# Performance work log

Measured on AMD Instinct MI355X. Metric: run time of the kernel, lower is better.

Reference implementation:

```python
import jax, jax.numpy as jnp
import numpy as np
from jax import lax

N = 120000      # total real voxels
C = 128         # d_model
NH = 8          # heads
HD = C // NH    # head dim
T = 36          # window capacity
FILL = 24       # real tokens per window
NW = N // FILL  # 5000 windows
L = 4           # encoder layers (num_blocks=2, 2 layers each)
DFF = 256
B, H, Wd = 2, 320, 320
SCALE = HD ** -0.5


def setup_inputs() -> dict:
    key = jax.random.key(0)
    ks = jax.random.split(key, 16)
    voxel_feats = jax.random.normal(ks[0], (N, C), jnp.float32)
    # shift-0 window assignment: contiguous; shift-1: random permutation of voxels
    base = jnp.arange(N, dtype=jnp.int32)
    ind0 = (base // FILL) * T + (base % FILL)
    perm = jax.random.permutation(ks[1], N).astype(jnp.int32)
    ind1 = (perm // FILL) * T + (perm % FILL)
    mask = jnp.tile(jnp.arange(T) >= FILL, (NW, 1))  # True = padded key slot
    pos0 = 0.02 * jax.random.normal(ks[2], (NW, T, C), jnp.float32)
    pos1 = 0.02 * jax.random.normal(ks[3], (NW, T, C), jnp.float32)
    bcol = (jnp.arange(N) >= N // 2).astype(jnp.int32)
    yy = jax.random.randint(ks[4], (N,), 0, H, jnp.int32)
    xx = jax.random.randint(ks[5], (N,), 0, Wd, jnp.int32)
    voxel_coors = jnp.stack([bcol, jnp.zeros(N, jnp.int32), yy, xx], axis=1)
    s = 0.02
    return dict(
        voxel_feats=voxel_feats,
        pos0=pos0, pos1=pos1,
        in_proj_w=s * jax.random.normal(ks[6], (L, 3 * C, C), jnp.float32),
        in_proj_b=jnp.zeros((L, 3 * C), jnp.float32),
        out_proj_w=s * jax.random.normal(ks[7], (L, C, C), jnp.float32),
        out_proj_b=jnp.zeros((L, C), jnp.float32),
        lin1_w=s * jax.random.normal(ks[8], (L, DFF, C), jnp.float32),
        lin1_b=jnp.zeros((L, DFF), jnp.float32),
        lin2_w=s * jax.random.normal(ks[9], (L, C, DFF), jnp.float32),
        lin2_b=jnp.zeros((L, C), jnp.float32),
        ln1_w=jnp.ones((L, C), jnp.float32), ln1_b=jnp.zeros((L, C), jnp.float32),
        ln2_w=jnp.ones((L, C), jnp.float32), ln2_b=jnp.zeros((L, C), jnp.float32),
        conv_w=0.05 * jax.random.normal(ks[10], (2, C, C, 3, 3), jnp.float32),
        voxel_coors=voxel_coors, ind0=ind0, ind1=ind1, mask0=mask, mask1=mask,
    )


def _ln(x, w, b):
    m = jnp.mean(x, -1, keepdims=True)
    v = jnp.mean((x - m) ** 2, -1, keepdims=True)
    return (x - m) * lax.rsqrt(v + 1e-5) * w + b


def _encoder_layer(x, ind, pos, mask, ipw, ipb, opw, opb, l1w, l1b, l2w, l2b,
                   n1w, n1b, n2w, n2b):
    # flat2window_v2: scatter flat tokens into padded window buffer
    feat3d = jnp.zeros((NW * T, C), x.dtype).at[ind].set(x).reshape(NW, T, C)
    qk_in = feat3d + pos  # pos added to q and k only
    wq, wk, wv = ipw[:C], ipw[C:2 * C], ipw[2 * C:]
    bq, bk, bv = ipb[:C], ipb[C:2 * C], ipb[2 * C:]
    q = (qk_in @ wq.T + bq).reshape(NW, T, NH, HD)
    k = (qk_in @ wk.T + bk).reshape(NW, T, NH, HD)
    v = (feat3d @ wv.T + bv).reshape(NW, T, NH, HD)
    scores = jnp.einsum('wqhd,wkhd->whqk', q, k) * SCALE
    scores = jnp.where(mask[:, None, None, :], -1e9, scores)  # key padding mask
    attn = jax.nn.softmax(scores, axis=-1)
    o = jnp.einsum('whqk,wkhd->wqhd', attn, v).reshape(NW, T, C)
    o = o @ opw.T + opb
    a = o.reshape(NW * T, C)[ind]  # window2flat_v2: gather valid slots
    x = _ln(x + a, n1w, n1b)       # post_norm residual 1
    f = jax.nn.gelu(x @ l1w.T + l1b, approximate=False) @ l2w.T + l2b
    return _ln(x + f, n2w, n2b)    # post_norm residual 2


def reference(voxel_feats, pos0, pos1, in_proj_w, in_proj_b, out_proj_w,
              out_proj_b, lin1_w, lin1_b, lin2_w, lin2_b, ln1_w, ln1_b,
              ln2_w, ln2_b, conv_w, voxel_coors, ind0, ind1, mask0, mask1):
    x = voxel_feats
    for l in range(L):
        ind, pos, mask = (ind0, pos0, mask0) if l % 2 == 0 else (ind1, pos1, mask1)
        x = _encoder_layer(x, ind, pos, mask, in_proj_w[l], in_proj_b[l],
                           out_proj_w[l], out_proj_b[l], lin1_w[l], lin1_b[l],
                           lin2_w[l], lin2_b[l], ln1_w[l], ln1_b[l],
                           ln2_w[l], ln2_b[l])
    # recover_bev: scatter tokens into dense [B, C, H, W] canvas
    flat = voxel_coors[:, 2] * Wd + voxel_coors[:, 3]
    canvas = jnp.zeros((B, H * Wd, C), x.dtype).at[voxel_coors[:, 0], flat].set(x)
    out = canvas.reshape(B, H, Wd, C).transpose(0, 3, 1, 2)
    for i in range(2):  # attached 3x3 conv (bias=False) + ReLU
        out = jax.nn.relu(lax.conv_general_dilated(
            out, conv_w[i], (1, 1), [(1, 1), (1, 1)],
            dimension_numbers=('NCHW', 'OIHW', 'NCHW')))
    return out
```

## Files before the change

### kernel.cpp

```cpp
#include <hip/hip_runtime.h>
#include <math.h>

#define NVOX 120000
#define CDIM 128
#define NWIN 5000
#define HWPIX 102400
#define PW 322
#define PCELLS 103684

typedef __attribute__((ext_vector_type(8))) short short8;
typedef __attribute__((ext_vector_type(4))) float f32x4;

__device__ __forceinline__ unsigned short f2bf(float f) {
  unsigned u = __float_as_uint(f);
  return (unsigned short)((u + 0x7FFFu + ((u >> 16) & 1u)) >> 16);
}
__device__ __forceinline__ unsigned pack2(float a, float b) {
  return (unsigned)f2bf(a) | ((unsigned)f2bf(b) << 16);
}
__device__ __forceinline__ void unpack2(unsigned u, float& a, float& b) {
  a = __uint_as_float(u << 16);
  b = __uint_as_float(u & 0xFFFF0000u);
}

__device__ __forceinline__ void mma128(const short* __restrict__ As,
                                       const short* __restrict__ Ws,
                                       int aoff, int boff, f32x4 acc[2][4]) {
#pragma unroll
  for (int kc = 0; kc < 4; ++kc) {
    short8 a0 = *(const short8*)(As + aoff + kc * 32);
    short8 a1 = *(const short8*)(As + aoff + 136 * 16 + kc * 32);
#pragma unroll
    for (int nt = 0; nt < 4; ++nt) {
      short8 b = *(const short8*)(Ws + boff + nt * 136 * 16 + kc * 32);
      acc[0][nt] = __builtin_amdgcn_mfma_f32_16x16x32_bf16(a0, b, acc[0][nt], 0, 0, 0);
      acc[1][nt] = __builtin_amdgcn_mfma_f32_16x16x32_bf16(a1, b, acc[1][nt], 0, 0, 0);
    }
  }
}

__global__ __launch_bounds__(256) void cvt_kernel(const float* __restrict__ src,
                                                  unsigned short* __restrict__ dst, int n4) {
  int i = blockIdx.x * 256 + threadIdx.x;
  if (i >= n4) return;
  float4 v = ((const float4*)src)[i];
  uint2 o; o.x = pack2(v.x, v.y); o.y = pack2(v.z, v.w);
  ((uint2*)dst)[i] = o;
}

__global__ __launch_bounds__(256) void cvtT_kernel(const float* __restrict__ w,
                                                   unsigned short* __restrict__ wT) {
  int idx = blockIdx.x * 256 + threadIdx.x;
  if (idx >= 2 * 9 * 128 * 128) return;
  int ci = idx & 127;
  int co = (idx >> 7) & 127;
  int tap = (idx >> 14) % 9;
  int conv = idx / (9 * 16384);
  wT[idx] = f2bf(w[((size_t)(conv * 128 + co) * 128 + ci) * 9 + tap]);
}

__global__ __launch_bounds__(256) void qkv_kernel(
    const unsigned short* __restrict__ x, const float* __restrict__ pos,
    const int* __restrict__ ind, const unsigned short* __restrict__ ipwB,
    const float* __restrict__ ipb, unsigned short* __restrict__ qb,
    unsigned short* __restrict__ kb, unsigned short* __restrict__ vb) {
  __shared__ __align__(16) char ldsraw[52224];
  short* As = (short*)ldsraw;
  short* Ws = (short*)(ldsraw + 17408);
  const int t = threadIdx.x;
  const int lane = t & 63, wv = t >> 6;
  const int l15 = lane & 15, quad = lane >> 4;
  const int rbase = 32 * (wv >> 1), cbase = 64 * (wv & 1);
  const int mbase = blockIdx.x * 64;
  const int sec = blockIdx.y;
  f32x4 acc[2][4];
#pragma unroll
  for (int m = 0; m < 2; ++m)
#pragma unroll
    for (int n = 0; n < 4; ++n) acc[m][n] = (f32x4){0.f, 0.f, 0.f, 0.f};

  for (int fi = t; fi < 1024; fi += 256) {
    int row = fi >> 4, c8 = fi & 15;
    int vox = mbase + row;
    uint4 xv = ((const uint4*)x)[(size_t)vox * 16 + c8];
    if (sec < 2) {
      int s = ind[vox];
      const float4* pp = (const float4*)(pos + (size_t)s * 128 + c8 * 8);
      float4 p0 = pp[0], p1 = pp[1];
      float f0, f1, f2, f3, f4, f5, f6, f7;
      unpack2(xv.x, f0, f1); unpack2(xv.y, f2, f3);
      unpack2(xv.z, f4, f5); unpack2(xv.w, f6, f7);
      xv.x = pack2(f0 + p0.x, f1 + p0.y); xv.y = pack2(f2 + p0.z, f3 + p0.w);
      xv.z = pack2(f4 + p1.x, f5 + p1.y); xv.w = pack2(f6 + p1.z, f7 + p1.w);
    }
    *(uint4*)&As[row * 136 + c8 * 8] = xv;
  }
  for (int fi = t; fi < 2048; fi += 256) {
    int row = fi >> 4, c8 = fi & 15;
    ((uint4*)&Ws[row * 136])[c8] =
        ((const uint4*)(ipwB + (size_t)(sec * 128 + row) * 128))[c8];
  }
  __syncthreads();
  mma128(As, Ws, (rbase + l15) * 136 + quad * 8, (cbase + l15) * 136 + quad * 8, acc);
  __syncthreads();

  short* Ybf = (short*)ldsraw;
#pragma unroll
  for (int nt = 0; nt < 4; ++nt) {
    int col = cbase + nt * 16 + l15;
    float bias = ipb[sec * 128 + col];
#pragma unroll
    for (int mt = 0; mt < 2; ++mt)
#pragma unroll
      for (int r = 0; r < 4; ++r)
        Ybf[(rbase + mt * 16 + quad * 4 + r) * 136 + col] =
            (short)f2bf(acc[mt][nt][r] + bias);
  }
  __syncthreads();
  unsigned short* dst = (sec == 0) ? qb : ((sec == 1) ? kb : vb);
  for (int fi = t; fi < 1024; fi += 256) {
    int row = fi >> 4, c8 = fi & 15;
    int s = ind[mbase + row];
    int slot = (s / 36) * 24 + (s % 36);
    ((uint4*)dst)[(size_t)slot * 16 + c8] = ((const uint4*)&Ybf[row * 136])[c8];
  }
}

__global__ __launch_bounds__(256) void attn_kernel(
    unsigned short* __restrict__ qb, const unsigned short* __restrict__ kb,
    const unsigned short* __restrict__ vb) {
  __shared__ float lds[14112];
  float* Qs = lds;
  float* Ks = lds + 3168;
  float* Vs = lds + 6336;
  float* S = lds + 9504;
  const int t = threadIdx.x;
  const size_t base = (size_t)blockIdx.x * 3072;
  for (int fi = t; fi < 1152; fi += 256) {
    int arr = fi / 384, rem = fi % 384;
    int row = rem >> 4, c8 = rem & 15;
    const unsigned short* src = arr == 0 ? qb : (arr == 1 ? kb : vb);
    uint4 raw = ((const uint4*)(src + base))[row * 16 + c8];
    float* dl = lds + arr * 3168 + row * 132 + c8 * 8;
    unpack2(raw.x, dl[0], dl[1]); unpack2(raw.y, dl[2], dl[3]);
    unpack2(raw.z, dl[4], dl[5]); unpack2(raw.w, dl[6], dl[7]);
  }
  __syncthreads();
  for (int idx = t; idx < 4608; idx += 256) {
    int hh = idx / 576, rem = idx % 576;
    int qq = rem / 24, kk = rem % 24;
    const float* qp = &Qs[qq * 132 + hh * 16];
    const float* kp = &Ks[kk * 132 + hh * 16];
    float s = 0.f;
#pragma unroll
    for (int d = 0; d < 16; ++d) s = fmaf(qp[d], kp[d], s);
    S[idx] = s * 0.25f;
  }
  __syncthreads();
  if (t < 192) {
    float* rowp = &S[t * 24];
    float m = rowp[0];
#pragma unroll
    for (int k2 = 1; k2 < 24; ++k2) m = fmaxf(m, rowp[k2]);
    float sum = 0.f;
#pragma unroll
    for (int k2 = 0; k2 < 24; ++k2) { float e = __expf(rowp[k2] - m); rowp[k2] = e; sum += e; }
    float inv = 1.f / sum;
#pragma unroll
    for (int k2 = 0; k2 < 24; ++k2) rowp[k2] *= inv;
  }
  __syncthreads();
  for (int idx = t; idx < 3072; idx += 256) {
    int hh = idx / 384, rem = idx % 384;
    int qq = rem >> 4, dd = rem & 15;
    const float* pp = &S[hh * 576 + qq * 24];
    const float* vp = &Vs[hh * 16 + dd];
    float o = 0.f;
#pragma unroll
    for (int k2 = 0; k2 < 24; ++k2) o = fmaf(pp[k2], vp[k2 * 132], o);
    qb[base + qq * 128 + hh * 16 + dd] = f2bf(o);
  }
}

__global__ __launch_bounds__(256) void outln_kernel(
    const unsigned short* __restrict__ o, const int* __restrict__ ind,
    const unsigned short* __restrict__ opwB, const float* __restrict__ opb,
    const unsigned short* __restrict__ xres, const float* __restrict__ lnw,
    const float* __restrict__ lnb, unsigned short* __restrict__ hout) {
  __shared__ __align__(16) char ldsraw[52224];
  short* As = (short*)ldsraw;
  short* Ws = (short*)(ldsraw + 17408);
  const int t = threadIdx.x;
  const int lane = t & 63, wv = t >> 6;
  const int l15 = lane & 15, quad = lane >> 4;
  const int rbase = 32 * (wv >> 1), cbase = 64 * (wv & 1);
  const int mbase = blockIdx.x * 64;
  f32x4 acc[2][4];
#pragma unroll
  for (int m = 0; m < 2; ++m)
#pragma unroll
    for (int n = 0; n < 4; ++n) acc[m][n] = (f32x4){0.f, 0.f, 0.f, 0.f};

  for (int fi = t; fi < 1024; fi += 256) {
    int row = fi >> 4, c8 = fi & 15;
    int s = ind[mbase + row];
    int slot = (s / 36) * 24 + (s % 36);
    *(uint4*)&As[row * 136 + c8 * 8] = ((const uint4*)o)[(size_t)slot * 16 + c8];
  }
  for (int fi = t; fi < 2048; fi += 256) {
    int row = fi >> 4, c8 = fi & 15;
    ((uint4*)&Ws[row * 136])[c8] = ((const uint4*)(opwB + (size_t)row * 128))[c8];
  }
  __syncthreads();
  mma128(As, Ws, (rbase + l15) * 136 + quad * 8, (cbase + l15) * 136 + quad * 8, acc);
  __syncthreads();

  float* Yf = (float*)ldsraw;
  float* p1 = (float*)(ldsraw + 33792);
  float* p2 = (float*)(ldsraw + 34816);
  float* Ms = (float*)(ldsraw + 35840);
  float* Rs = (float*)(ldsraw + 36096);
#pragma unroll
  for (int nt = 0; nt < 4; ++nt) {
    int col = cbase + nt * 16 + l15;
    float bias = opb[col];
#pragma unroll
    for (int mt = 0; mt < 2; ++mt)
#pragma unroll
      for (int r = 0; r < 4; ++r)
        Yf[(rbase + mt * 16 + quad * 4 + r) * 132 + col] = acc[mt][nt][r] + bias;
  }
  __syncthreads();
  for (int fi = t; fi < 1024; fi += 256) {
    int row = fi >> 4, c8 = fi & 15;
    uint4 xv = ((const uint4*)xres)[(size_t)(mbase + row) * 16 + c8];
    float* yp = &Yf[row * 132 + c8 * 8];
    float a, b;
    unpack2(xv.x, a, b); yp[0] += a; yp[1] += b;
    unpack2(xv.y, a, b); yp[2] += a; yp[3] += b;
    unpack2(xv.z, a, b); yp[4] += a; yp[5] += b;
    unpack2(xv.w, a, b); yp[6] += a; yp[7] += b;
  }
  __syncthreads();
  {
    int r = t & 63, g = t >> 6;
    float s = 0.f, s2 = 0.f;
    for (int c = g * 32; c < g * 32 + 32; ++c) { float v = Yf[r * 132 + c]; s += v; s2 += v * v; }
    p1[g * 64 + r] = s; p2[g * 64 + r] = s2;
  }
  __syncthreads();
  if (t < 64) {
    float s = p1[t] + p1[64 + t] + p1[128 + t] + p1[192 + t];
    float s2 = p2[t] + p2[64 + t] + p2[128 + t] + p2[192 + t];
    float m = s * (1.f / 128.f);
    float var = s2 * (1.f / 128.f) - m * m;
    Ms[t] = m; Rs[t] = rsqrtf(var + 1e-5f);
  }
  __syncthreads();
  for (int fi = t; fi < 1024; fi += 256) {
    int row = fi >> 4, c8 = fi & 15;
    float m = Ms[row], rr = Rs[row];
    const float* yp = &Yf[row * 132 + c8 * 8];
    uint4 ov;
    float v0, v1;
#define LNPAIR(J, FLD) \
    v0 = (yp[2*J] - m) * rr * lnw[c8*8+2*J] + lnb[c8*8+2*J]; \
    v1 = (yp[2*J+1] - m) * rr * lnw[c8*8+2*J+1] + lnb[c8*8+2*J+1]; \
    ov.FLD = pack2(v0, v1);
    LNPAIR(0, x) LNPAIR(1, y) LNPAIR(2, z) LNPAIR(3, w)
#undef LNPAIR
    ((uint4*)hout)[(size_t)(mbase + row) * 16 + c8] = ov;
  }
}

__global__ __launch_bounds__(256) void ffn1_kernel(
    const unsigned short* __restrict__ h, const unsigned short* __restrict__ w1B,
    const float* __restrict__ b1, unsigned short* __restrict__ ff) {
  __shared__ __align__(16) char ldsraw[52224];
  short* As = (short*)ldsraw;
  short* Ws = (short*)(ldsraw + 17408);
  const int t = threadIdx.x;
  const int lane = t & 63, wv = t >> 6;
  const int l15 = lane & 15, quad = lane >> 4;
  const int rbase = 32 * (wv >> 1), cbase = 64 * (wv & 1);
  const int mbase = blockIdx.x * 64;
  const int by = blockIdx.y;
  f32x4 acc[2][4];
#pragma unroll
  for (int m = 0; m < 2; ++m)
#pragma unroll
    for (int n = 0; n < 4; ++n) acc[m][n] = (f32x4){0.f, 0.f, 0.f, 0.f};

  for (int fi = t; fi < 1024; fi += 256) {
    int row = fi >> 4, c8 = fi & 15;
    *(uint4*)&As[row * 136 + c8 * 8] = ((const uint4*)h)[(size_t)(mbase + row) * 16 + c8];
  }
  for (int fi = t; fi < 2048; fi += 256) {
    int row = fi >> 4, c8 = fi & 15;
    ((uint4*)&Ws[row * 136])[c8] =
        ((const uint4*)(w1B + (size_t)(by * 128 + row) * 128))[c8];
  }
  __syncthreads();
  mma128(As, Ws, (rbase + l15) * 136 + quad * 8, (cbase + l15) * 136 + quad * 8, acc);
  __syncthreads();

  short* Ybf = (short*)ldsraw;
#pragma unroll
  for (int nt = 0; nt < 4; ++nt) {
    int col = cbase + nt * 16 + l15;
    float bias = b1[by * 128 + col];
#pragma unroll
    for (int mt = 0; mt < 2; ++mt)
#pragma unroll
      for (int r = 0; r < 4; ++r) {
        float v = acc[mt][nt][r] + bias;
        float g = 0.5f * v * (1.f + erff(v * 0.70710678f));
        Ybf[(rbase + mt * 16 + quad * 4 + r) * 136 + col] = (short)f2bf(g);
      }
  }
  __syncthreads();
  for (int fi = t; fi < 1024; fi += 256) {
    int row = fi >> 4, c8 = fi & 15;
    ((uint4*)ff)[(size_t)(mbase + row) * 32 + by * 16 + c8] =
        ((const uint4*)&Ybf[row * 136])[c8];
  }
}

__global__ __launch_bounds__(256) void ffn2_kernel(
    const unsigned short* __restrict__ ff, const unsigned short* __restrict__ w2B,
    const float* __restrict__ b2, const unsigned short* __restrict__ hres,
    const float* __restrict__ lnw, const float* __restrict__ lnb,
    unsigned short* __restrict__ xout) {
  __shared__ __align__(16) char ldsraw[52224];
  short* As = (short*)ldsraw;
  short* Ws = (short*)(ldsraw + 17408);
  const int t = threadIdx.x;
  const int lane = t & 63, wv = t >> 6;
  const int l15 = lane & 15, quad = lane >> 4;
  const int rbase = 32 * (wv >> 1), cbase = 64 * (wv & 1);
  const int mbase = blockIdx.x * 64;
  f32x4 acc[2][4];
#pragma unroll
  for (int m = 0; m < 2; ++m)
#pragma unroll
    for (int n = 0; n < 4; ++n) acc[m][n] = (f32x4){0.f, 0.f, 0.f, 0.f};

  for (int k2 = 0; k2 < 2; ++k2) {
    if (k2) __syncthreads();
    for (int fi = t; fi < 1024; fi += 256) {
      int row = fi >> 4, c8 = fi & 15;
      *(uint4*)&As[row * 136 + c8 * 8] =
          ((const uint4*)ff)[(size_t)(mbase + row) * 32 + k2 * 16 + c8];
    }
    for (int fi = t; fi < 2048; fi += 256) {
      int row = fi >> 4, c8 = fi & 15;
      ((uint4*)&Ws[row * 136])[c8] =
          ((const uint4*)(w2B + (size_t)row * 256 + k2 * 128))[c8];
    }
    __syncthreads();
    mma128(As, Ws, (rbase + l15) * 136 + quad * 8, (cbase + l15) * 136 + quad * 8, acc);
  }
  __syncthreads();

  float* Yf = (float*)ldsraw;
  float* p1 = (float*)(ldsraw + 33792);
  float* p2 = (float*)(ldsraw + 34816);
  float* Ms = (float*)(ldsraw + 35840);
  float* Rs = (float*)(ldsraw + 36096);
#pragma unroll
  for (int nt = 0; nt < 4; ++nt) {
    int col = cbase + nt * 16 + l15;
    float bias = b2[col];
#pragma unroll
    for (int mt = 0; mt < 2; ++mt)
#pragma unroll
      for (int r = 0; r < 4; ++r)
        Yf[(rbase + mt * 16 + quad * 4 + r) * 132 + col] = acc[mt][nt][r] + bias;
  }
  __syncthreads();
  for (int fi = t; fi < 1024; fi += 256) {
    int row = fi >> 4, c8 = fi & 15;
    uint4 xv = ((const uint4*)hres)[(size_t)(mbase + row) * 16 + c8];
    float* yp = &Yf[row * 132 + c8 * 8];
    float a, b;
    unpack2(xv.x, a, b); yp[0] += a; yp[1] += b;
    unpack2(xv.y, a, b); yp[2] += a; yp[3] += b;
    unpack2(xv.z, a, b); yp[4] += a; yp[5] += b;
    unpack2(xv.w, a, b); yp[6] += a; yp[7] += b;
  }
  __syncthreads();
  {
    int r = t & 63, g = t >> 6;
    float s = 0.f, s2 = 0.f;
    for (int c = g * 32; c < g * 32 + 32; ++c) { float v = Yf[r * 132 + c]; s += v; s2 += v * v; }
    p1[g * 64 + r] = s; p2[g * 64 + r] = s2;
  }
  __syncthreads();
  if (t < 64) {
    float s = p1[t] + p1[64 + t] + p1[128 + t] + p1[192 + t];
    float s2 = p2[t] + p2[64 + t] + p2[128 + t] + p2[192 + t];
    float m = s * (1.f / 128.f);
    float var = s2 * (1.f / 128.f) - m * m;
    Ms[t] = m; Rs[t] = rsqrtf(var + 1e-5f);
  }
  __syncthreads();
  for (int fi = t; fi < 1024; fi += 256) {
    int row = fi >> 4, c8 = fi & 15;
    float m = Ms[row], rr = Rs[row];
    const float* yp = &Yf[row * 132 + c8 * 8];
    uint4 ov;
    float v0, v1;
#define LNPAIR(J, FLD) \
    v0 = (yp[2*J] - m) * rr * lnw[c8*8+2*J] + lnb[c8*8+2*J]; \
    v1 = (yp[2*J+1] - m) * rr * lnw[c8*8+2*J+1] + lnb[c8*8+2*J+1]; \
    ov.FLD = pack2(v0, v1);
    LNPAIR(0, x) LNPAIR(1, y) LNPAIR(2, z) LNPAIR(3, w)
#undef LNPAIR
    ((uint4*)xout)[(size_t)(mbase + row) * 16 + c8] = ov;
  }
}

__global__ void idx_init_kernel(int* __restrict__ idxmap) {
  int i = blockIdx.x * 256 + threadIdx.x;
  if (i < 2 * HWPIX) idxmap[i] = -1;
}

__global__ void scatter_kernel(const int* __restrict__ coors, int* __restrict__ idxmap) {
  int i = blockIdx.x * 256 + threadIdx.x;
  if (i >= NVOX) return;
  int b = coors[i * 4 + 0], y = coors[i * 4 + 2], xx = coors[i * 4 + 3];
  atomicMax(&idxmap[b * HWPIX + y * 320 + xx], i);
}

__global__ void canvas_kernel(const unsigned short* __restrict__ x,
                              const int* __restrict__ idxmap,
                              unsigned short* __restrict__ canvas) {
  int idx = blockIdx.x * 256 + threadIdx.x;
  if (idx >= 2 * PCELLS * 16) return;
  int cell = idx >> 4, c8 = idx & 15;
  int b = (cell >= PCELLS) ? 1 : 0;
  cell -= b * PCELLS;
  int yy = cell / PW, xx = cell - yy * PW;
  uint4 v = {0u, 0u, 0u, 0u};
  if (yy >= 1 && yy <= 320 && xx >= 1 && xx <= 320) {
    int vox = idxmap[b * HWPIX + (yy - 1) * 320 + (xx - 1)];
    if (vox >= 0) v = ((const uint4*)x)[(size_t)vox * 16 + c8];
  }
  ((uint4*)canvas)[idx] = v;
}

__global__ void border_kernel(unsigned short* __restrict__ buf) {
  int i = blockIdx.x * 256 + threadIdx.x;
  if (i >= 2 * 1284 * 16) return;
  int c8 = i & 15, j = i >> 4;
  int b = (j >= 1284) ? 1 : 0;
  j -= b * 1284;
  int cell;
  if (j < 322) cell = j;
  else if (j < 644) cell = 321 * PW + (j - 322);
  else { int j2 = j - 644; cell = (1 + (j2 >> 1)) * PW + (j2 & 1) * 321; }
  uint4 z = {0u, 0u, 0u, 0u};
  ((uint4*)buf)[((size_t)b * PCELLS + cell) * 16 + c8] = z;
}

template <int NCHW_OUT>
__global__ __launch_bounds__(256) void conv_kernel(
    const unsigned short* __restrict__ in, const unsigned short* __restrict__ wTb,
    void* __restrict__ outp) {
  __shared__ __align__(16) char ldsraw[67584];
  const int t = threadIdx.x;
  const int lane = t & 63, wv = t >> 6;
  const int l15 = lane & 15, quad = lane >> 4;
  const int wr = wv >> 1, wc = wv & 1;
  const int x0 = blockIdx.x * 64;
  const int y0 = blockIdx.y * 2;
  const int b = blockIdx.z;
  const unsigned short* inb = in + (size_t)b * PCELLS * 128;
  const int srow = t >> 4, sc8 = t & 15;

  f32x4 acc[4][4];
#pragma unroll
  for (int m = 0; m < 4; ++m)
#pragma unroll
    for (int n = 0; n < 4; ++n) acc[m][n] = (f32x4){0.f, 0.f, 0.f, 0.f};

  uint4 wreg[8];
#pragma unroll
  for (int i = 0; i < 8; ++i)
    wreg[i] = ((const uint4*)(wTb + (size_t)(i * 16 + srow) * 128))[sc8];
  {
    short* W0 = (short*)ldsraw;
#pragma unroll
    for (int i = 0; i < 8; ++i)
      *(uint4*)&W0[(i * 16 + srow) * 132 + sc8 * 8] = wreg[i];
  }
  __syncthreads();

#pragma unroll
  for (int tap = 0; tap < 9; ++tap) {
    const int dy = tap / 3, dx = tap % 3;
    const short* Wcur = (const short*)(ldsraw + (tap & 1) * 33792);
    if (tap < 8) {
#pragma unroll
      for (int i = 0; i < 8; ++i)
        wreg[i] = ((const uint4*)(wTb + (size_t)((tap + 1) * 128 + i * 16 + srow) * 128))[sc8];
    }
    const unsigned short* ap =
        inb + (size_t)((y0 + wr + dy) * PW + x0 + dx + l15) * 128 + quad * 8;
    const short* bp = Wcur + (wc * 64 + l15) * 132 + quad * 8;
#pragma unroll
    for (int kc = 0; kc < 4; ++kc) {
      short8 av[4], bvv[4];
#pragma unroll
      for (int mt = 0; mt < 4; ++mt)
        av[mt] = *(const short8*)(ap + mt * 16 * 128 + kc * 32);
#pragma unroll
      for (int nt = 0; nt < 4; ++nt)
        bvv[nt] = *(const short8*)(bp + nt * 16 * 132 + kc * 32);
#pragma unroll
      for (int mt = 0; mt < 4; ++mt)
#pragma unroll
        for (int nt = 0; nt < 4; ++nt)
          acc[mt][nt] = __builtin_amdgcn_mfma_f32_16x16x32_bf16(av[mt], bvv[nt], acc[mt][nt], 0, 0, 0);
    }
    if (tap < 8) {
      short* Wnxt = (short*)(ldsraw + ((tap + 1) & 1) * 33792);
#pragma unroll
      for (int i = 0; i < 8; ++i)
        *(uint4*)&Wnxt[(i * 16 + srow) * 132 + sc8 * 8] = wreg[i];
      __syncthreads();
    }
  }
  __syncthreads();

  if (NCHW_OUT) {
    float* Yf = (float*)ldsraw;
#pragma unroll
    for (int nt = 0; nt < 4; ++nt) {
      int co = wc * 64 + nt * 16 + l15;
#pragma unroll
      for (int mt = 0; mt < 4; ++mt)
#pragma unroll
        for (int r = 0; r < 4; ++r)
          Yf[co * 129 + wr * 64 + mt * 16 + quad * 4 + r] = fmaxf(acc[mt][nt][r], 0.f);
    }
    __syncthreads();
    float* out = (float*)outp;
    for (int fi = t; fi < 4096; fi += 256) {
      int co = fi >> 5, q4 = fi & 31;
      int px = q4 * 4;
      int yy = y0 + (px >> 6), xx = x0 + (px & 63);
      *(float4*)&out[(size_t)(b * 128 + co) * HWPIX + yy * 320 + xx] =
          *(const float4*)&Yf[co * 129 + px];
    }
  } else {
    short* Ybf = (short*)ldsraw;
#pragma unroll
    for (int nt = 0; nt < 4; ++nt) {
      int co = wc * 64 + nt * 16 + l15;
#pragma unroll
      for (int mt = 0; mt < 4; ++mt)
#pragma unroll
        for (int r = 0; r < 4; ++r)
          Ybf[(wr * 64 + mt * 16 + quad * 4 + r) * 132 + co] =
              (short)f2bf(fmaxf(acc[mt][nt][r], 0.f));
    }
    __syncthreads();
    unsigned short* out = (unsigned short*)outp;
    for (int fi = t; fi < 2048; fi += 256) {
      int row = fi >> 4, c8 = fi & 15;
      int yy = y0 + (row >> 6) + 1, xx = x0 + (row & 63) + 1;
      ((uint4*)out)[((size_t)b * PCELLS + yy * PW + xx) * 16 + c8] =
          ((const uint4*)&Ybf[row * 132])[c8];
    }
  }
}

extern "C" void kernel_launch(void* const* d_in, const int* in_sizes, int n_in,
                              void* d_out, int out_size, void* d_ws, size_t ws_size,
                              hipStream_t stream) {
  const float* voxel_feats = (const float*)d_in[0];
  const float* pos0 = (const float*)d_in[1];
  const float* pos1 = (const float*)d_in[2];
  const float* ipw = (const float*)d_in[3];
  const float* ipb = (const float*)d_in[4];
  const float* opw = (const float*)d_in[5];
  const float* opb = (const float*)d_in[6];
  const float* l1w = (const float*)d_in[7];
  const float* l1b = (const float*)d_in[8];
  const float* l2w = (const float*)d_in[9];
  const float* l2b = (const float*)d_in[10];
  const float* n1w = (const float*)d_in[11];
  const float* n1b = (const float*)d_in[12];
  const float* n2w = (const float*)d_in[13];
  const float* n2b = (const float*)d_in[14];
  const float* convw = (const float*)d_in[15];
  const int* coors = (const int*)d_in[16];
  const int* ind0 = (const int*)d_in[17];
  const int* ind1 = (const int*)d_in[18];

  unsigned short* ws = (unsigned short*)d_ws;
  const size_t NC = (size_t)NVOX * CDIM;
  unsigned short* bx = ws;
  unsigned short* bq = ws + NC;
  unsigned short* bk = ws + 2 * NC;
  unsigned short* bv = ws + 3 * NC;
  unsigned short* bh = ws + 4 * NC;
  unsigned short* bff = ws + 5 * NC;
  unsigned short* wB = ws + 7 * NC;
  unsigned short* ipwB = wB;
  unsigned short* opwB = wB + 196608;
  unsigned short* l1wB = wB + 262144;
  unsigned short* l2wB = wB + 393216;
  unsigned short* convB = wB + 524288;
  int* idxmap = (int*)(wB + 819200);
  unsigned short* canvas = bq;
  unsigned short* c1out = bv;

  cvt_kernel<<<15000, 256, 0, stream>>>(voxel_feats, bx, 3840000);
  cvt_kernel<<<192, 256, 0, stream>>>(ipw, ipwB, 49152);
  cvt_kernel<<<64, 256, 0, stream>>>(opw, opwB, 16384);
  cvt_kernel<<<128, 256, 0, stream>>>(l1w, l1wB, 32768);
  cvt_kernel<<<128, 256, 0, stream>>>(l2w, l2wB, 32768);
  cvtT_kernel<<<1152, 256, 0, stream>>>(convw, convB);

  for (int l = 0; l < 4; ++l) {
    const int* ind = (l & 1) ? ind1 : ind0;
    const float* pos = (l & 1) ? pos1 : pos0;
    qkv_kernel<<<dim3(1875, 3), 256, 0, stream>>>(
        bx, pos, ind, ipwB + (size_t)l * 49152, ipb + l * 384, bq, bk, bv);
    attn_kernel<<<NWIN, 256, 0, stream>>>(bq, bk, bv);
    outln_kernel<<<1875, 256, 0, stream>>>(
        bq, ind, opwB + (size_t)l * 16384, opb + l * 128, bx,
        n1w + l * 128, n1b + l * 128, bh);
    ffn1_kernel<<<dim3(1875, 2), 256, 0, stream>>>(
        bh, l1wB + (size_t)l * 32768, l1b + l * 256, bff);
    ffn2_kernel<<<1875, 256, 0, stream>>>(
        bff, l2wB + (size_t)l * 32768, l2b + l * 128, bh,
        n2w + l * 128, n2b + l * 128, bx);
  }

  idx_init_kernel<<<800, 256, 0, stream>>>(idxmap);
  scatter_kernel<<<(NVOX + 255) / 256, 256, 0, stream>>>(coors, idxmap);
  canvas_kernel<<<(2 * PCELLS * 16 + 255) / 256, 256, 0, stream>>>(bx, idxmap, canvas);
  border_kernel<<<(2 * 1284 * 16 + 255) / 256, 256, 0, stream>>>(c1out);

  conv_kernel<0><<<dim3(5, 160, 2), 256, 0, stream>>>(canvas, convB, (void*)c1out);
  conv_kernel<1><<<dim3(5, 160, 2), 256, 0, stream>>>(c1out, convB + 9 * 16384, d_out);
}
```

Baseline: 1.759 ms.

## Stage conv input row patch in LDS and tile one output row per block

The 3x3 conv kernel now loads a 66-pixel input row patch into shared memory and reuses it across the three horizontal taps, refreshing it only when the tap row changes. Before, A operands were read straight from global memory for every tap. Each block now covers one output row instead of two, and the grid doubles. Weights move to a single LDS buffer, so an extra barrier is needed per tap. The cost is more blocks that each redo the weight loading, which halves weight reuse per block. The diff calls an mma128 helper that it does not show being defined.

```diff
diff --git a/kernel.cpp b/kernel.cpp
--- a/kernel.cpp
+++ b/kernel.cpp
@@ -467,111 +467,119 @@
 __global__ __launch_bounds__(256) void conv_kernel(
     const unsigned short* __restrict__ in, const unsigned short* __restrict__ wTb,
     void* __restrict__ outp) {
-  __shared__ __align__(16) char ldsraw[67584];
+  __shared__ __align__(16) char ldsraw[52768];
+  short* patch = (short*)ldsraw;
+  short* Wt = (short*)(ldsraw + 17952);
   const int t = threadIdx.x;
   const int lane = t & 63, wv = t >> 6;
   const int l15 = lane & 15, quad = lane >> 4;
-  const int wr = wv >> 1, wc = wv & 1;
+  const int rbase = 32 * (wv >> 1), cbase = 64 * (wv & 1);
   const int x0 = blockIdx.x * 64;
-  const int y0 = blockIdx.y * 2;
+  const int y0 = blockIdx.y;
   const int b = blockIdx.z;
   const unsigned short* inb = in + (size_t)b * PCELLS * 128;
   const int srow = t >> 4, sc8 = t & 15;
 
-  f32x4 acc[4][4];
-#pragma unroll
-  for (int m = 0; m < 4; ++m)
+  f32x4 acc[2][4];
+#pragma unroll
+  for (int m = 0; m < 2; ++m)
 #pragma unroll
     for (int n = 0; n < 4; ++n) acc[m][n] = (f32x4){0.f, 0.f, 0.f, 0.f};
 
   uint4 wreg[8];
+  uint4 pp[4], px4;
+
+  {
+    const uint4* src = (const uint4*)inb + ((size_t)y0 * PW + x0) * 16;
+#pragma unroll
+    for (int k = 0; k < 4; ++k) pp[k] = src[t + 256 * k];
+    if (t < 32) px4 = src[1024 + t];
+  }
 #pragma unroll
   for (int i = 0; i < 8; ++i)
     wreg[i] = ((const uint4*)(wTb + (size_t)(i * 16 + srow) * 128))[sc8];
-  {
-    short* W0 = (short*)ldsraw;
-#pragma unroll
-    for (int i = 0; i < 8; ++i)
-      *(uint4*)&W0[(i * 16 + srow) * 132 + sc8 * 8] = wreg[i];
-  }
+#pragma unroll
+  for (int k = 0; k < 4; ++k) {
+    int e = t + 256 * k;
+    *(uint4*)&patch[(e >> 4) * 136 + (e & 15) * 8] = pp[k];
+  }
+  if (t < 32) { int e = 1024 + t; *(uint4*)&patch[(e >> 4) * 136 + (e & 15) * 8] = px4; }
+#pragma unroll
+  for (int i = 0; i < 8; ++i)
+    *(uint4*)&Wt[(i * 16 + srow) * 136 + sc8 * 8] = wreg[i];
   __syncthreads();
 
 #pragma unroll
   for (int tap = 0; tap < 9; ++tap) {
     const int dy = tap / 3, dx = tap % 3;
-    const short* Wcur = (const short*)(ldsraw + (tap & 1) * 33792);
-    if (tap < 8) {
+    const bool pfP = (dx == 2) && (dy < 2);
+    const bool pfW = (tap < 8);
+    if (pfP) {
+      const uint4* src = (const uint4*)inb + ((size_t)(y0 + dy + 1) * PW + x0) * 16;
+#pragma unroll
+      for (int k = 0; k < 4; ++k) pp[k] = src[t + 256 * k];
+      if (t < 32) px4 = src[1024 + t];
+    }
+    if (pfW) {
 #pragma unroll
       for (int i = 0; i < 8; ++i)
         wreg[i] = ((const uint4*)(wTb + (size_t)((tap + 1) * 128 + i * 16 + srow) * 128))[sc8];
     }
-    const unsigned short* ap =
-        inb + (size_t)((y0 + wr + dy) * PW + x0 + dx + l15) * 128 + quad * 8;
-    const short* bp = Wcur + (wc * 64 + l15) * 132 + quad * 8;
-#pragma unroll
-    for (int kc = 0; kc < 4; ++kc) {
-      short8 av[4], bvv[4];
-#pragma unroll
-      for (int mt = 0; mt < 4; ++mt)
-        av[mt] = *(const short8*)(ap + mt * 16 * 128 + kc * 32);
-#pragma unroll
-      for (int nt = 0; nt < 4; ++nt)
-        bvv[nt] = *(const short8*)(bp + nt * 16 * 132 + kc * 32);
-#pragma unroll
-      for (int mt = 0; mt < 4; ++mt)
-#pragma unroll
-        for (int nt = 0; nt < 4; ++nt)
-          acc[mt][nt] = __builtin_amdgcn_mfma_f32_16x16x32_bf16(av[mt], bvv[nt], acc[mt][nt], 0, 0, 0);
-    }
-    if (tap < 8) {
-      short* Wnxt = (short*)(ldsraw + ((tap + 1) & 1) * 33792);
+    mma128(patch, Wt, (rbase + l15 + dx) * 136 + quad * 8,
+           (cbase + l15) * 136 + quad * 8, acc);
+    __syncthreads();
+    if (pfW) {
+      if (pfP) {
+#pragma unroll
+        for (int k = 0; k < 4; ++k) {
+          int e = t + 256 * k;
+          *(uint4*)&patch[(e >> 4) * 136 + (e & 15) * 8] = pp[k];
+        }
+        if (t < 32) { int e = 1024 + t; *(uint4*)&patch[(e >> 4) * 136 + (e & 15) * 8] = px4; }
+      }
 #pragma unroll
       for (int i = 0; i < 8; ++i)
-        *(uint4*)&Wnxt[(i * 16 + srow) * 132 + sc8 * 8] = wreg[i];
+        *(uint4*)&Wt[(i * 16 + srow) * 136 + sc8 * 8] = wreg[i];
       __syncthreads();
     }
   }
-  __syncthreads();
 
   if (NCHW_OUT) {
     float* Yf = (float*)ldsraw;
 #pragma unroll
     for (int nt = 0; nt < 4; ++nt) {
-      int co = wc * 64 + nt * 16 + l15;
-#pragma unroll
-      for (int mt = 0; mt < 4; ++mt)
+      int col = cbase + nt * 16 + l15;
+#pragma unroll
+      for (int mt = 0; mt < 2; ++mt)
 #pragma unroll
         for (int r = 0; r < 4; ++r)
-          Yf[co * 129 + wr * 64 + mt * 16 + quad * 4 + r] = fmaxf(acc[mt][nt][r], 0.f);
+          Yf[col * 68 + rbase + mt * 16 + quad * 4 + r] = fmaxf(acc[mt][nt][r], 0.f);
     }
     __syncthreads();
     float* out = (float*)outp;
-    for (int fi = t; fi < 4096; fi += 256) {
-      int co = fi >> 5, q4 = fi & 31;
-      int px = q4 * 4;
-      int yy = y0 + (px >> 6), xx = x0 + (px & 63);
-      *(float4*)&out[(size_t)(b * 128 + co) * HWPIX + yy * 320 + xx] =
-          *(const float4*)&Yf[co * 129 + px];
+    for (int fi = t; fi < 2048; fi += 256) {
+      int co = fi >> 4, q4 = fi & 15;
+      float4 v = *(float4*)&Yf[co * 68 + q4 * 4];
+      *(float4*)&out[(size_t)(b * 128 + co) * HWPIX + y0 * 320 + x0 + q4 * 4] = v;
     }
   } else {
     short* Ybf = (short*)ldsraw;
 #pragma unroll
     for (int nt = 0; nt < 4; ++nt) {
-      int co = wc * 64 + nt * 16 + l15;
-#pragma unroll
-      for (int mt = 0; mt < 4; ++mt)
+      int col = cbase + nt * 16 + l15;
+#pragma unroll
+      for (int mt = 0; mt < 2; ++mt)
 #pragma unroll
         for (int r = 0; r < 4; ++r)
-          Ybf[(wr * 64 + mt * 16 + quad * 4 + r) * 132 + co] =
+          Ybf[(rbase + mt * 16 + quad * 4 + r) * 136 + col] =
               (short)f2bf(fmaxf(acc[mt][nt][r], 0.f));
     }
     __syncthreads();
     unsigned short* out = (unsigned short*)outp;
-    for (int fi = t; fi < 2048; fi += 256) {
+    for (int fi = t; fi < 1024; fi += 256) {
       int row = fi >> 4, c8 = fi & 15;
-      int yy = y0 + (row >> 6) + 1, xx = x0 + (row & 63) + 1;
-      ((uint4*)out)[((size_t)b * PCELLS + yy * PW + xx) * 16 + c8] =
-          ((const uint4*)&Ybf[row * 132])[c8];
+      ((uint4*)out)[((size_t)b * PCELLS + (size_t)(y0 + 1) * PW + x0 + 1 + row) * 16 + c8] =
+          ((const uint4*)&Ybf[row * 136])[c8];
     }
   }
 }
@@ -645,6 +653,6 @@
   canvas_kernel<<<(2 * PCELLS * 16 + 255) / 256, 256, 0, stream>>>(bx, idxmap, canvas);
   border_kernel<<<(2 * 1284 * 16 + 255) / 256, 256, 0, stream>>>(c1out);
 
-  conv_kernel<0><<<dim3(5, 160, 2), 256, 0, stream>>>(canvas, convB, (void*)c1out);
-  conv_kernel<1><<<dim3(5, 160, 2), 256, 0, stream>>>(c1out, convB + 9 * 16384, d_out);
-}
+  conv_kernel<0><<<dim3(5, 320, 2), 256, 0, stream>>>(canvas, convB, (void*)c1out);
+  conv_kernel<1><<<dim3(5, 320, 2), 256, 0, stream>>>(c1out, convB + 9 * 16384, d_out);
+}
```

Measured after the change: 1.949 ms. 10.8% more time.
